# Kernel optimization log

Measured on AMD Instinct MI355X. Metric: run time of the kernel, lower is better.

## Reference

```python
import jax, jax.numpy as jnp
import numpy as np

B, NPG, F, HOPS, OUT = 1024, 128, 128, 3, 32  # graphs, nodes/graph, feat, hops, output_dim
DEG = 16  # average degree


def setup_inputs() -> dict:
    key = jax.random.key(0)
    k = jax.random.split(key, 10)
    N = B * NPG
    X = jax.random.normal(k[0], (N, F), jnp.float32)
    batch = jnp.repeat(jnp.arange(B, dtype=jnp.int32), NPG)
    # per-graph random undirected edges (both directions), offset into global ids
    eh = NPG * DEG // 2  # undirected edges per graph
    src = jax.random.randint(k[1], (B * eh,), 0, NPG)
    dst = jax.random.randint(k[2], (B * eh,), 0, NPG)
    off = jnp.repeat(jnp.arange(B, dtype=jnp.int32), eh) * NPG
    u, v = src + off, dst + off
    edge_index = jnp.stack([jnp.concatenate([u, v]), jnp.concatenate([v, u])]).astype(jnp.int32)
    s1 = 1.0 / np.sqrt(F * (HOPS + 1))
    W1 = jax.random.normal(k[3], (HOPS + 1, F, F), jnp.float32) * s1
    b1 = jnp.zeros((F,), jnp.float32)
    W2 = jax.random.normal(k[4], (HOPS + 1, F, F), jnp.float32) * s1
    b2 = jnp.zeros((F,), jnp.float32)
    W_out = jax.random.normal(k[5], (F, OUT), jnp.float32) * (1.0 / np.sqrt(F))
    b_out = jnp.zeros((OUT,), jnp.float32)
    alpha = jnp.float32(0.5)
    return dict(X=X, W1=W1, b1=b1, W2=W2, b2=b2, W_out=W_out, b_out=b_out,
                alpha=alpha, batch=batch, edge_index=edge_index)


def _filters(adj, alpha, hops):
    # hub-normalized GSO: S = D^{-alpha} A D^{alpha-1}  (sym-norm at alpha=0.5)
    deg = adj.sum(-1)                                   # [B, n]
    ds = jnp.where(deg > 0, deg, 1.0)
    S = (ds ** (-alpha))[:, :, None] * adj * (ds ** (alpha - 1.0))[:, None, :]
    n = adj.shape[-1]
    eye = jnp.broadcast_to(jnp.eye(n, dtype=adj.dtype), S.shape)
    filt = [eye]
    for _ in range(hops):
        filt.append(filt[-1] @ S)
    return jnp.stack(filt)                              # [K, B, n, n]


def reference(X, W1, b1, W2, b2, W_out, b_out, alpha, batch, edge_index):
    N, Fd = X.shape
    nb = int(batch[-1]) + 1          # number of graphs (equal-sized)
    n = N // nb                      # nodes per graph
    ei = edge_index.astype(jnp.int32)
    g, u, v = ei[0] // n, ei[0] % n, ei[1] % n
    adj = jnp.zeros((nb, n, n), X.dtype).at[g, u, v].set(1.0)  # dense per-graph adjacency
    Sk = _filters(adj, alpha, HOPS)                             # [K, B, n, n]
    h = X.reshape(nb, n, Fd)
    h = jax.nn.relu(jnp.einsum('kbij,bjf,kfo->bio', Sk, h, W1) + b1)
    h = jax.nn.relu(jnp.einsum('kbij,bjf,kfo->bio', Sk, h, W2) + b2)
    pooled = h.max(axis=1)           # global max pool over nodes -> [B, F]
    return pooled @ W_out + b_out    # [B, OUT]
```

## Files before the change

### kernel.cpp

```cpp
#include <hip/hip_runtime.h>
#include <cstdint>
#include <cstddef>

#define NGRAPH 1024
#define NPGX   128
#define FDIM   128
#define KTAPS  4
#define ODIM   32
#define ZROW   136

typedef _Float16 half_t;
typedef __attribute__((ext_vector_type(8))) _Float16 half8;
typedef __attribute__((ext_vector_type(4))) _Float16 half4v;
typedef __attribute__((ext_vector_type(4))) float f32x4;

__global__ __launch_bounds__(256) void edge_scatter(const int* __restrict__ ei,
                                                    uint32_t* __restrict__ bits,
                                                    int E) {
    int e = blockIdx.x * blockDim.x + threadIdx.x;
    if (e >= E) return;
    int u = ei[e];
    int v = ei[E + e];
    int lv = v & (NPGX - 1);
    atomicOr(bits + ((size_t)u << 2) + (lv >> 5), 1u << (lv & 31));
}

__global__ __launch_bounds__(256) void wtrans(const float* __restrict__ W1,
                                              const float* __restrict__ W2,
                                              half_t* __restrict__ WT) {
    __shared__ float ld[32][132];
    const int b  = blockIdx.x;
    const int lk = b >> 2;
    const int f0 = (b & 3) * 32;
    const float* W = (lk < 4 ? W1 : W2) + (size_t)(lk & 3) * FDIM * FDIM;
    const int t = threadIdx.x;
    #pragma unroll
    for (int i = 0; i < 4; i++) {
        int e4 = t + i * 256;
        int fr = e4 >> 5, c4 = (e4 & 31) * 4;
        float4 v = *(const float4*)&W[(size_t)(f0 + fr) * FDIM + c4];
        ld[fr][c4 + 0] = v.x; ld[fr][c4 + 1] = v.y;
        ld[fr][c4 + 2] = v.z; ld[fr][c4 + 3] = v.w;
    }
    __syncthreads();
    const int o = t >> 1, seg = (t & 1) * 16;
    half_t tmp[16];
    #pragma unroll
    for (int j = 0; j < 16; j++) tmp[j] = (half_t)ld[seg + j][o];
    half8* dst = (half8*)&WT[((size_t)lk * FDIM + o) * FDIM + f0 + seg];
    dst[0] = *(half8*)&tmp[0];
    dst[1] = *(half8*)&tmp[8];
}

__global__ __launch_bounds__(512) void gcnn_fused(
    const float* __restrict__ X,
    const float* __restrict__ b1, const float* __restrict__ b2,
    const float* __restrict__ Wout, const float* __restrict__ bout,
    const float* __restrict__ alphap,
    const uint32_t* __restrict__ bits,
    const half_t* __restrict__ WT,
    float* __restrict__ out)
{
    __shared__ half_t Zs[NPGX * ZROW];
    __shared__ half_t Zt[NPGX * ZROW];
    __shared__ half_t Ss[NPGX * ZROW];
    __shared__ uint32_t adj[NPGX][4];
    __shared__ float dsl[NPGX], dsr[NPGX];
    __shared__ float biasL[2][FDIM];
    __shared__ float pooled[FDIM];
    __shared__ float ppart[8][ODIM];

    const int g    = blockIdx.x;
    const int t    = threadIdx.x;
    const int lane = t & 63;
    const int w    = t >> 6;
    const int lg   = lane >> 4;
    const int lr   = lane & 15;

    adj[t >> 2][t & 3] = bits[(size_t)g * 512 + t];
    if (t < 256) biasL[t >> 7][t & 127] = (t < 128 ? b1[t] : b2[t & 127]);

    {
        const float4* Xs = (const float4*)(X + (size_t)g * NPGX * FDIM);
        #pragma unroll
        for (int i = 0; i < 8; i++) {
            int e4 = t + i * 512;
            int r = e4 >> 5, c0 = (e4 & 31) * 4;
            float4 v = Xs[e4];
            half_t h0 = (half_t)v.x, h1 = (half_t)v.y,
                   h2 = (half_t)v.z, h3 = (half_t)v.w;
            half4v hv = {h0, h1, h2, h3};
            *(half4v*)&Zs[r * ZROW + c0] = hv;
            Zt[(c0 + 0) * ZROW + r] = h0;
            Zt[(c0 + 1) * ZROW + r] = h1;
            Zt[(c0 + 2) * ZROW + r] = h2;
            Zt[(c0 + 3) * ZROW + r] = h3;
        }
    }
    __syncthreads();

    if (t < NPGX) {
        int d = __popc(adj[t][0]) + __popc(adj[t][1]) +
                __popc(adj[t][2]) + __popc(adj[t][3]);
        float ds = d > 0 ? (float)d : 1.0f;
        float a = alphap[0];
        dsl[t] = powf(ds, -a);
        dsr[t] = powf(ds, a - 1.0f);
    }
    __syncthreads();

    {
        int row = t >> 2, c0 = (t & 3) * 32;
        float dl = dsl[row];
        #pragma unroll
        for (int cc = 0; cc < 32; cc += 8) {
            half_t tmp[8];
            #pragma unroll
            for (int j = 0; j < 8; j++) {
                int c = c0 + cc + j;
                uint32_t m = adj[row][c >> 5];
                float s = ((m >> (c & 31)) & 1u) ? dl * dsr[c] : 0.f;
                tmp[j] = (half_t)s;
            }
            *(half8*)&Ss[row * ZROW + c0 + cc] = *(half8*)tmp;
        }
    }
    __syncthreads();

    for (int layer = 0; layer < 2; layer++) {
        f32x4 accW[8];
        #pragma unroll
        for (int i = 0; i < 8; i++) accW[i] = (f32x4){0.f, 0.f, 0.f, 0.f};

        for (int k = 0; k < KTAPS; k++) {
            const half_t* wtp = WT + ((size_t)(layer * 4 + k) * FDIM + (w * 16 + lr)) * FDIM;
            half8 aW0 = *(const half8*)&wtp[0 * 32 + lg * 8];
            half8 aW1 = *(const half8*)&wtp[1 * 32 + lg * 8];
            half8 aW2 = *(const half8*)&wtp[2 * 32 + lg * 8];
            half8 aW3 = *(const half8*)&wtp[3 * 32 + lg * 8];

            #pragma unroll
            for (int tl = 0; tl < 8; tl++) {
                const half_t* zrow = &Zs[(tl * 16 + lr) * ZROW + lg * 8];
                accW[tl] = __builtin_amdgcn_mfma_f32_16x16x32_f16(aW0, *(const half8*)&zrow[0],  accW[tl], 0, 0, 0);
                accW[tl] = __builtin_amdgcn_mfma_f32_16x16x32_f16(aW1, *(const half8*)&zrow[32], accW[tl], 0, 0, 0);
                accW[tl] = __builtin_amdgcn_mfma_f32_16x16x32_f16(aW2, *(const half8*)&zrow[64], accW[tl], 0, 0, 0);
                accW[tl] = __builtin_amdgcn_mfma_f32_16x16x32_f16(aW3, *(const half8*)&zrow[96], accW[tl], 0, 0, 0);
            }

            if (k < KTAPS - 1) {
                const half_t* srow = &Ss[(w * 16 + lr) * ZROW + lg * 8];
                half8 aS0 = *(const half8*)&srow[0];
                half8 aS1 = *(const half8*)&srow[32];
                half8 aS2 = *(const half8*)&srow[64];
                half8 aS3 = *(const half8*)&srow[96];
                f32x4 dp[8];
                #pragma unroll
                for (int i = 0; i < 8; i++) dp[i] = (f32x4){0.f, 0.f, 0.f, 0.f};
                #pragma unroll
                for (int tl = 0; tl < 8; tl++) {
                    const half_t* ztr = &Zt[(tl * 16 + lr) * ZROW + lg * 8];
                    dp[tl] = __builtin_amdgcn_mfma_f32_16x16x32_f16(aS0, *(const half8*)&ztr[0],  dp[tl], 0, 0, 0);
                    dp[tl] = __builtin_amdgcn_mfma_f32_16x16x32_f16(aS1, *(const half8*)&ztr[32], dp[tl], 0, 0, 0);
                    dp[tl] = __builtin_amdgcn_mfma_f32_16x16x32_f16(aS2, *(const half8*)&ztr[64], dp[tl], 0, 0, 0);
                    dp[tl] = __builtin_amdgcn_mfma_f32_16x16x32_f16(aS3, *(const half8*)&ztr[96], dp[tl], 0, 0, 0);
                }
                __syncthreads();
                #pragma unroll
                for (int tl = 0; tl < 8; tl++) {
                    #pragma unroll
                    for (int r = 0; r < 4; r++) {
                        int i = w * 16 + lg * 4 + r;
                        int f = tl * 16 + lr;
                        half_t h = (half_t)dp[tl][r];
                        Zs[i * ZROW + f] = h;
                        Zt[f * ZROW + i] = h;
                    }
                }
                __syncthreads();
            }
        }

        if (layer == 0) {
            __syncthreads();
            #pragma unroll
            for (int tl = 0; tl < 8; tl++) {
                #pragma unroll
                for (int r = 0; r < 4; r++) {
                    int o = w * 16 + lg * 4 + r;
                    int i = tl * 16 + lr;
                    float v = fmaxf(accW[tl][r] + biasL[0][o], 0.f);
                    half_t h = (half_t)v;
                    Zs[i * ZROW + o] = h;
                    Zt[o * ZROW + i] = h;
                }
            }
            __syncthreads();
        } else {
            float pm[4];
            #pragma unroll
            for (int r = 0; r < 4; r++) {
                float bv = biasL[1][w * 16 + lg * 4 + r];
                float v = 0.f;
                #pragma unroll
                for (int tl = 0; tl < 8; tl++)
                    v = fmaxf(v, fmaxf(accW[tl][r] + bv, 0.f));
                #pragma unroll
                for (int m = 1; m < 16; m <<= 1)
                    v = fmaxf(v, __shfl_xor(v, m, 64));
                pm[r] = v;
            }
            if (lr == 0) {
                #pragma unroll
                for (int r = 0; r < 4; r++)
                    pooled[w * 16 + lg * 4 + r] = pm[r];
            }
        }
    }
    __syncthreads();

    if (t < 256) {
        int o = t & 31, seg = t >> 5;
        float s = 0.f;
        #pragma unroll
        for (int j = 0; j < 16; j++) {
            int f = seg * 16 + j;
            s = fmaf(pooled[f], Wout[f * ODIM + o], s);
        }
        ppart[seg][o] = s;
    }
    __syncthreads();
    if (t < ODIM) {
        float s = bout[t];
        #pragma unroll
        for (int j = 0; j < 8; j++) s += ppart[j][t];
        out[(size_t)g * ODIM + t] = s;
    }
}

extern "C" void kernel_launch(void* const* d_in, const int* in_sizes, int n_in,
                              void* d_out, int out_size, void* d_ws, size_t ws_size,
                              hipStream_t stream) {
    const float* X    = (const float*)d_in[0];
    const float* W1   = (const float*)d_in[1];
    const float* b1   = (const float*)d_in[2];
    const float* W2   = (const float*)d_in[3];
    const float* b2   = (const float*)d_in[4];
    const float* Wout = (const float*)d_in[5];
    const float* bout = (const float*)d_in[6];
    const float* alph = (const float*)d_in[7];
    const int*   ei   = (const int*)d_in[9];

    const int E = in_sizes[9] / 2;

    half_t*   WT   = (half_t*)d_ws;
    uint32_t* bits = (uint32_t*)((char*)d_ws + 2 * 4 * FDIM * FDIM * sizeof(half_t));
    const size_t bits_bytes = (size_t)NGRAPH * NPGX * 4 * sizeof(uint32_t);

    hipMemsetAsync(bits, 0, bits_bytes, stream);

    wtrans<<<32, 256, 0, stream>>>(W1, W2, WT);
    edge_scatter<<<(E + 255) / 256, 256, 0, stream>>>(ei, bits, E);

    gcnn_fused<<<NGRAPH, 512, 0, stream>>>(X, b1, b2, Wout, bout, alph,
                                           bits, WT, (float*)d_out);
}
```

Baseline: 269.3 us.

## Fuse edge scatter into main kernel, swizzle LDS, retile MFMA warps 2D

Adjacency bit construction moves into the fused kernel, using shared-memory atomics on per-graph edge ranges. This drops the global memset and the separate scatter kernel. The padded LDS layout is replaced by an XOR-swizzled 128-wide layout, and the S matrix is held in registers instead of shared memory, which cuts LDS use so more blocks fit per CU (launch bounds 512,4). Warps are retiled as 4x2 over 32x64 output tiles so each B fragment is reused across two A fragments. The in-kernel scatter assumes edges are laid out contiguously per graph, with the forward half followed by the reverse half.

```diff
diff --git a/kernel.cpp b/kernel.cpp
--- a/kernel.cpp
+++ b/kernel.cpp
@@ -5,24 +5,15 @@
 #define NGRAPH 1024
 #define NPGX   128
 #define FDIM   128
-#define KTAPS  4
 #define ODIM   32
-#define ZROW   136
 
 typedef _Float16 half_t;
 typedef __attribute__((ext_vector_type(8))) _Float16 half8;
 typedef __attribute__((ext_vector_type(4))) _Float16 half4v;
 typedef __attribute__((ext_vector_type(4))) float f32x4;
 
-__global__ __launch_bounds__(256) void edge_scatter(const int* __restrict__ ei,
-                                                    uint32_t* __restrict__ bits,
-                                                    int E) {
-    int e = blockIdx.x * blockDim.x + threadIdx.x;
-    if (e >= E) return;
-    int u = ei[e];
-    int v = ei[E + e];
-    int lv = v & (NPGX - 1);
-    atomicOr(bits + ((size_t)u << 2) + (lv >> 5), 1u << (lv & 31));
+__device__ __forceinline__ int zaddr(int row, int col) {
+    return row * 128 + ((((col >> 3) ^ (row & 7)) << 3) | (col & 7));
 }
 
 __global__ __launch_bounds__(256) void wtrans(const float* __restrict__ W1,
@@ -52,33 +43,44 @@
     dst[1] = *(half8*)&tmp[8];
 }
 
-__global__ __launch_bounds__(512) void gcnn_fused(
+__global__ __launch_bounds__(512, 4) void gcnn_fused(
     const float* __restrict__ X,
     const float* __restrict__ b1, const float* __restrict__ b2,
     const float* __restrict__ Wout, const float* __restrict__ bout,
     const float* __restrict__ alphap,
-    const uint32_t* __restrict__ bits,
+    const int* __restrict__ ei, int E,
     const half_t* __restrict__ WT,
     float* __restrict__ out)
 {
-    __shared__ half_t Zs[NPGX * ZROW];
-    __shared__ half_t Zt[NPGX * ZROW];
-    __shared__ half_t Ss[NPGX * ZROW];
+    __shared__ half_t Zs[NPGX * 128];
+    __shared__ half_t Zt[NPGX * 128];
     __shared__ uint32_t adj[NPGX][4];
     __shared__ float dsl[NPGX], dsr[NPGX];
     __shared__ float biasL[2][FDIM];
-    __shared__ float pooled[FDIM];
+    __shared__ float pooled2[2][FDIM];
     __shared__ float ppart[8][ODIM];
 
-    const int g    = blockIdx.x;
-    const int t    = threadIdx.x;
-    const int lane = t & 63;
-    const int w    = t >> 6;
-    const int lg   = lane >> 4;
-    const int lr   = lane & 15;
-
-    adj[t >> 2][t & 3] = bits[(size_t)g * 512 + t];
-    if (t < 256) biasL[t >> 7][t & 127] = (t < 128 ? b1[t] : b2[t & 127]);
+    const int g  = blockIdx.x;
+    const int t  = threadIdx.x;
+    const int l  = t & 63;
+    const int w  = t >> 6;
+    const int wm = w >> 1;
+    const int wn = w & 1;
+    const int lg = l >> 4;
+    const int lr = l & 15;
+
+    ((uint32_t*)adj)[t] = 0;
+    __syncthreads();
+
+    const int ehg = E / 2 / NGRAPH;
+    for (int e = t; e < ehg; e += 512) {
+        int e1 = g * ehg + e;
+        int u1 = ei[e1] & 127, v1 = ei[E + e1] & 127;
+        atomicOr(&adj[u1][v1 >> 5], 1u << (v1 & 31));
+        int e2 = E / 2 + g * ehg + e;
+        int u2 = ei[e2] & 127, v2 = ei[E + e2] & 127;
+        atomicOr(&adj[u2][v2 >> 5], 1u << (v2 & 31));
+    }
 
     {
         const float4* Xs = (const float4*)(X + (size_t)g * NPGX * FDIM);
@@ -87,14 +89,8 @@
             int e4 = t + i * 512;
             int r = e4 >> 5, c0 = (e4 & 31) * 4;
             float4 v = Xs[e4];
-            half_t h0 = (half_t)v.x, h1 = (half_t)v.y,
-                   h2 = (half_t)v.z, h3 = (half_t)v.w;
-            half4v hv = {h0, h1, h2, h3};
-            *(half4v*)&Zs[r * ZROW + c0] = hv;
-            Zt[(c0 + 0) * ZROW + r] = h0;
-            Zt[(c0 + 1) * ZROW + r] = h1;
-            Zt[(c0 + 2) * ZROW + r] = h2;
-            Zt[(c0 + 3) * ZROW + r] = h3;
+            half4v hv = { (half_t)v.x, (half_t)v.y, (half_t)v.z, (half_t)v.w };
+            *(half4v*)&Zs[zaddr(r, c0)] = hv;
         }
     }
     __syncthreads();
@@ -107,76 +103,98 @@
         dsl[t] = powf(ds, -a);
         dsr[t] = powf(ds, a - 1.0f);
     }
-    __syncthreads();
+    if (t < 256) biasL[t >> 7][t & 127] = (t < 128) ? b1[t] : b2[t & 127];
 
     {
-        int row = t >> 2, c0 = (t & 3) * 32;
-        float dl = dsl[row];
-        #pragma unroll
-        for (int cc = 0; cc < 32; cc += 8) {
-            half_t tmp[8];
-            #pragma unroll
-            for (int j = 0; j < 8; j++) {
-                int c = c0 + cc + j;
-                uint32_t m = adj[row][c >> 5];
-                float s = ((m >> (c & 31)) & 1u) ? dl * dsr[c] : 0.f;
-                tmp[j] = (half_t)s;
+        int f = t & 127, iseg = t >> 7;
+        half_t tmp[32];
+        #pragma unroll
+        for (int ii = 0; ii < 32; ii++)
+            tmp[ii] = Zs[zaddr(iseg * 32 + ii, f)];
+        __syncthreads();
+        #pragma unroll
+        for (int s = 0; s < 4; s++)
+            *(half8*)&Zt[zaddr(f, iseg * 32 + s * 8)] = *(half8*)&tmp[s * 8];
+    }
+
+    half8 sfr[2][4];
+    {
+        #pragma unroll
+        for (int ms = 0; ms < 2; ms++) {
+            int i = wm * 32 + ms * 16 + lr;
+            float dli = dsl[i];
+            uint32_t a0 = adj[i][0], a1 = adj[i][1], a2 = adj[i][2], a3 = adj[i][3];
+            #pragma unroll
+            for (int ks = 0; ks < 4; ks++) {
+                half8 hv;
+                #pragma unroll
+                for (int jj = 0; jj < 8; jj++) {
+                    int j = ks * 32 + lg * 8 + jj;
+                    uint32_t word = (j < 32) ? a0 : (j < 64) ? a1 : (j < 96) ? a2 : a3;
+                    float s = ((word >> (j & 31)) & 1u) ? dli * dsr[j] : 0.f;
+                    hv[jj] = (half_t)s;
+                }
+                sfr[ms][ks] = hv;
             }
-            *(half8*)&Ss[row * ZROW + c0 + cc] = *(half8*)tmp;
-        }
-    }
-    __syncthreads();
-
+        }
+    }
+    __syncthreads();
+
+    #pragma unroll 1
     for (int layer = 0; layer < 2; layer++) {
-        f32x4 accW[8];
-        #pragma unroll
-        for (int i = 0; i < 8; i++) accW[i] = (f32x4){0.f, 0.f, 0.f, 0.f};
-
-        for (int k = 0; k < KTAPS; k++) {
-            const half_t* wtp = WT + ((size_t)(layer * 4 + k) * FDIM + (w * 16 + lr)) * FDIM;
-            half8 aW0 = *(const half8*)&wtp[0 * 32 + lg * 8];
-            half8 aW1 = *(const half8*)&wtp[1 * 32 + lg * 8];
-            half8 aW2 = *(const half8*)&wtp[2 * 32 + lg * 8];
-            half8 aW3 = *(const half8*)&wtp[3 * 32 + lg * 8];
-
-            #pragma unroll
-            for (int tl = 0; tl < 8; tl++) {
-                const half_t* zrow = &Zs[(tl * 16 + lr) * ZROW + lg * 8];
-                accW[tl] = __builtin_amdgcn_mfma_f32_16x16x32_f16(aW0, *(const half8*)&zrow[0],  accW[tl], 0, 0, 0);
-                accW[tl] = __builtin_amdgcn_mfma_f32_16x16x32_f16(aW1, *(const half8*)&zrow[32], accW[tl], 0, 0, 0);
-                accW[tl] = __builtin_amdgcn_mfma_f32_16x16x32_f16(aW2, *(const half8*)&zrow[64], accW[tl], 0, 0, 0);
-                accW[tl] = __builtin_amdgcn_mfma_f32_16x16x32_f16(aW3, *(const half8*)&zrow[96], accW[tl], 0, 0, 0);
+        f32x4 acc[2][4];
+        #pragma unroll
+        for (int ms = 0; ms < 2; ms++)
+            #pragma unroll
+            for (int nt = 0; nt < 4; nt++)
+                acc[ms][nt] = (f32x4){0.f, 0.f, 0.f, 0.f};
+
+        #pragma unroll 1
+        for (int k = 0; k < 4; k++) {
+            const half_t* wbase = WT + (size_t)(layer * 4 + k) * FDIM * FDIM;
+            #pragma unroll
+            for (int ks = 0; ks < 4; ks++) {
+                half8 a0 = *(const half8*)&wbase[(wm * 32 + 0  + lr) * 128 + ks * 32 + lg * 8];
+                half8 a1 = *(const half8*)&wbase[(wm * 32 + 16 + lr) * 128 + ks * 32 + lg * 8];
+                #pragma unroll
+                for (int nt = 0; nt < 4; nt++) {
+                    int iC = wn * 64 + nt * 16 + lr;
+                    half8 b = *(const half8*)&Zs[zaddr(iC, ks * 32 + lg * 8)];
+                    acc[0][nt] = __builtin_amdgcn_mfma_f32_16x16x32_f16(a0, b, acc[0][nt], 0, 0, 0);
+                    acc[1][nt] = __builtin_amdgcn_mfma_f32_16x16x32_f16(a1, b, acc[1][nt], 0, 0, 0);
+                }
             }
 
-            if (k < KTAPS - 1) {
-                const half_t* srow = &Ss[(w * 16 + lr) * ZROW + lg * 8];
-                half8 aS0 = *(const half8*)&srow[0];
-                half8 aS1 = *(const half8*)&srow[32];
-                half8 aS2 = *(const half8*)&srow[64];
-                half8 aS3 = *(const half8*)&srow[96];
-                f32x4 dp[8];
-                #pragma unroll
-                for (int i = 0; i < 8; i++) dp[i] = (f32x4){0.f, 0.f, 0.f, 0.f};
-                #pragma unroll
-                for (int tl = 0; tl < 8; tl++) {
-                    const half_t* ztr = &Zt[(tl * 16 + lr) * ZROW + lg * 8];
-                    dp[tl] = __builtin_amdgcn_mfma_f32_16x16x32_f16(aS0, *(const half8*)&ztr[0],  dp[tl], 0, 0, 0);
-                    dp[tl] = __builtin_amdgcn_mfma_f32_16x16x32_f16(aS1, *(const half8*)&ztr[32], dp[tl], 0, 0, 0);
-                    dp[tl] = __builtin_amdgcn_mfma_f32_16x16x32_f16(aS2, *(const half8*)&ztr[64], dp[tl], 0, 0, 0);
-                    dp[tl] = __builtin_amdgcn_mfma_f32_16x16x32_f16(aS3, *(const half8*)&ztr[96], dp[tl], 0, 0, 0);
-                }
+            if (k < 3) {
+                f32x4 dp[2][4];
+                #pragma unroll
+                for (int ms = 0; ms < 2; ms++)
+                    #pragma unroll
+                    for (int nt = 0; nt < 4; nt++)
+                        dp[ms][nt] = (f32x4){0.f, 0.f, 0.f, 0.f};
+                #pragma unroll
+                for (int ks = 0; ks < 4; ks++)
+                    #pragma unroll
+                    for (int nt = 0; nt < 4; nt++) {
+                        int fC = wn * 64 + nt * 16 + lr;
+                        half8 b = *(const half8*)&Zt[zaddr(fC, ks * 32 + lg * 8)];
+                        dp[0][nt] = __builtin_amdgcn_mfma_f32_16x16x32_f16(sfr[0][ks], b, dp[0][nt], 0, 0, 0);
+                        dp[1][nt] = __builtin_amdgcn_mfma_f32_16x16x32_f16(sfr[1][ks], b, dp[1][nt], 0, 0, 0);
+                    }
                 __syncthreads();
                 #pragma unroll
-                for (int tl = 0; tl < 8; tl++) {
-                    #pragma unroll
-                    for (int r = 0; r < 4; r++) {
-                        int i = w * 16 + lg * 4 + r;
-                        int f = tl * 16 + lr;
-                        half_t h = (half_t)dp[tl][r];
-                        Zs[i * ZROW + f] = h;
-                        Zt[f * ZROW + i] = h;
+                for (int ms = 0; ms < 2; ms++)
+                    #pragma unroll
+                    for (int nt = 0; nt < 4; nt++) {
+                        int fC = wn * 64 + nt * 16 + lr;
+                        int i0 = wm * 32 + ms * 16 + lg * 4;
+                        half4v hv = { (half_t)dp[ms][nt][0], (half_t)dp[ms][nt][1],
+                                      (half_t)dp[ms][nt][2], (half_t)dp[ms][nt][3] };
+                        *(half4v*)&Zt[zaddr(fC, i0)] = hv;
+                        #pragma unroll
+                        for (int r = 0; r < 4; r++)
+                            Zs[zaddr(i0 + r, fC)] = hv[r];
                     }
-                }
                 __syncthreads();
             }
         }
@@ -184,37 +202,37 @@
         if (layer == 0) {
             __syncthreads();
             #pragma unroll
-            for (int tl = 0; tl < 8; tl++) {
-                #pragma unroll
-                for (int r = 0; r < 4; r++) {
-                    int o = w * 16 + lg * 4 + r;
-                    int i = tl * 16 + lr;
-                    float v = fmaxf(accW[tl][r] + biasL[0][o], 0.f);
-                    half_t h = (half_t)v;
-                    Zs[i * ZROW + o] = h;
-                    Zt[o * ZROW + i] = h;
-                }
-            }
+            for (int ms = 0; ms < 2; ms++)
+                #pragma unroll
+                for (int nt = 0; nt < 4; nt++) {
+                    int iC  = wn * 64 + nt * 16 + lr;
+                    int fo0 = wm * 32 + ms * 16 + lg * 4;
+                    half4v hv;
+                    #pragma unroll
+                    for (int r = 0; r < 4; r++)
+                        hv[r] = (half_t)fmaxf(acc[ms][nt][r] + biasL[0][fo0 + r], 0.f);
+                    *(half4v*)&Zs[zaddr(iC, fo0)] = hv;
+                    #pragma unroll
+                    for (int r = 0; r < 4; r++)
+                        Zt[zaddr(fo0 + r, iC)] = hv[r];
+                }
             __syncthreads();
         } else {
-            float pm[4];
-            #pragma unroll
-            for (int r = 0; r < 4; r++) {
-                float bv = biasL[1][w * 16 + lg * 4 + r];
-                float v = 0.f;
-                #pragma unroll
-                for (int tl = 0; tl < 8; tl++)
-                    v = fmaxf(v, fmaxf(accW[tl][r] + bv, 0.f));
-                #pragma unroll
-                for (int m = 1; m < 16; m <<= 1)
-                    v = fmaxf(v, __shfl_xor(v, m, 64));
-                pm[r] = v;
-            }
-            if (lr == 0) {
-                #pragma unroll
-                for (int r = 0; r < 4; r++)
-                    pooled[w * 16 + lg * 4 + r] = pm[r];
-            }
+            #pragma unroll
+            for (int ms = 0; ms < 2; ms++)
+                #pragma unroll
+                for (int r = 0; r < 4; r++) {
+                    int fo = wm * 32 + ms * 16 + lg * 4 + r;
+                    float bv = biasL[1][fo];
+                    float v = 0.f;
+                    #pragma unroll
+                    for (int nt = 0; nt < 4; nt++)
+                        v = fmaxf(v, acc[ms][nt][r] + bv);
+                    #pragma unroll
+                    for (int m = 1; m < 16; m <<= 1)
+                        v = fmaxf(v, __shfl_xor(v, m, 64));
+                    if (lr == 0) pooled2[wn][fo] = v;
+                }
         }
     }
     __syncthreads();
@@ -225,7 +243,8 @@
         #pragma unroll
         for (int j = 0; j < 16; j++) {
             int f = seg * 16 + j;
-            s = fmaf(pooled[f], Wout[f * ODIM + o], s);
+            float p = fmaxf(pooled2[0][f], pooled2[1][f]);
+            s = fmaf(p, Wout[f * ODIM + o], s);
         }
         ppart[seg][o] = s;
     }
@@ -252,16 +271,10 @@
     const int*   ei   = (const int*)d_in[9];
 
     const int E = in_sizes[9] / 2;
-
-    half_t*   WT   = (half_t*)d_ws;
-    uint32_t* bits = (uint32_t*)((char*)d_ws + 2 * 4 * FDIM * FDIM * sizeof(half_t));
-    const size_t bits_bytes = (size_t)NGRAPH * NPGX * 4 * sizeof(uint32_t);
-
-    hipMemsetAsync(bits, 0, bits_bytes, stream);
+    half_t* WT = (half_t*)d_ws;
 
     wtrans<<<32, 256, 0, stream>>>(W1, W2, WT);
-    edge_scatter<<<(E + 255) / 256, 256, 0, stream>>>(ei, bits, E);
 
     gcnn_fused<<<NGRAPH, 512, 0, stream>>>(X, b1, b2, Wout, bout, alph,
-                                           bits, WT, (float*)d_out);
-}
+                                           ei, E, WT, (float*)d_out);
+}
```

Result: slower. 329.0 us (+22.1%).
